# Kernel tuning notes

Hardware: AMD Instinct MI355X
Metric: run time of the kernel (lower is better)

The kernel has to match this reference:

```python
import jax, jax.numpy as jnp
import numpy as np

D = 18          # belief dimension (max category dim)
EPS = 0.1       # C.eps
PROP_STEP = 5   # C.prop_step
CC = 0.01       # label-injection constant c in forward
DIM_A = 4       # category_dim_dict['author']
DIM_P = 18      # category_dim_dict['paper']


def _init_belief(mask, label, dim, d):
    # X[tr_idx] = -c everywhere, then X[tr_idx, label] += dim*c
    m = (mask != 0).astype(jnp.float32)[:, None]            # [N,1]
    X = -CC * m + (dim * CC) * m * jax.nn.one_hot(label, d, dtype=jnp.float32)
    col_mask = (jnp.arange(d) < dim).astype(jnp.float32)    # zero cols >= dim
    Y = X * col_mask
    return X, Y, col_mask


def setup_inputs() -> dict:
    key = jax.random.key(0)
    ks = jax.random.split(key, 8)
    E, NA, NP = 2_000_000, 100_000, 500_000
    return {
        "H_ap": jax.random.normal(ks[0], (D, D), dtype=jnp.float32),
        "H_pa": jax.random.normal(ks[1], (D, D), dtype=jnp.float32),
        "w": jnp.ones((E,), dtype=jnp.float32),
        "edge_src": jax.random.randint(ks[2], (E,), 0, NA, dtype=jnp.int32),
        "edge_dst": jax.random.randint(ks[3], (E,), 0, NP, dtype=jnp.int32),
        "train_mask_a": jax.random.randint(ks[4], (NA,), 0, 2, dtype=jnp.int32),
        "label_a": jax.random.randint(ks[5], (NA,), 0, DIM_A, dtype=jnp.int32),
        "train_mask_p": jax.random.randint(ks[6], (NP,), 0, 2, dtype=jnp.int32),
        "label_p": jax.random.randint(ks[7], (NP,), 0, DIM_P, dtype=jnp.int32),
        "n_author": NA,
        "n_paper": NP,
    }


def reference(H_ap, H_pa, w, edge_src, edge_dst, train_mask_a, label_a,
              train_mask_p, label_p, n_author, n_paper):
    # Belief init via scatter-based label injection (per node type)
    Xa, Ya, cm_a = _init_belief(train_mask_a, label_a, DIM_A, D)
    Xp, Yp, cm_p = _init_belief(train_mask_p, label_p, DIM_P, D)

    seg = jax.ops.segment_sum
    for _ in range(PROP_STEP):  # ZooBP residual updates over hetero edge types
        # author -> paper: gather, transform by H_ap, weighted scatter-add
        msg_p = seg(w[:, None] * (Ya[edge_src] @ H_ap), edge_dst,
                    num_segments=n_paper)                       # [NP, D]
        # paper -> author (inverse etype, H_pa ~ H_ap^T structure)
        msg_a = seg(w[:, None] * (Yp[edge_dst] @ H_pa), edge_src,
                    num_segments=n_author)                      # [NA, D]
        Ya = (Xa + (EPS / D) * msg_a) * cm_a
        Yp = (Xp + (EPS / D) * msg_p) * cm_p
    return Ya, Yp
```

## Files before the change

kernel.cpp:

```cpp
#include <hip/hip_runtime.h>


static constexpr int   DD     = 18;
static constexpr int   DIMA   = 4;
static constexpr float CCF    = 0.01f;
static constexpr float SCALEF = 0.1f / 18.0f;
static constexpr int   PROP   = 5;

static constexpr int NBLK  = 1024;
static constexpr int PBK   = 1024;
static constexpr int ABK   = 512;
static constexpr int NBIN  = PBK + ABK;
static constexpr int NBINS = NBIN * NBLK;

__device__ __forceinline__ float bf2f(unsigned short u) {
    return __uint_as_float(((unsigned int)u) << 16);
}
__device__ __forceinline__ unsigned short f2bf(float f) {
    unsigned int x = __float_as_uint(f);
    return (unsigned short)((x + 0x7fffu + ((x >> 16) & 1u)) >> 16);
}
__device__ __forceinline__ unsigned int f2w13(float f) {
    unsigned int x = __float_as_uint(f);
    return ((x + 0x3ffffu + ((x >> 19) & 1u)) >> 19) & 0x1fffu;
}
__device__ __forceinline__ float w132f(unsigned int u) {
    return __uint_as_float(u << 19);
}
__device__ __forceinline__ int swz_blk() {
    return ((int)blockIdx.x & 7) * (NBLK >> 3) + ((int)blockIdx.x >> 3);
}

__global__ __launch_bounds__(256) void count_bins(
    const int* __restrict__ esrc, const int* __restrict__ edst,
    int* __restrict__ bb, int E, int chunk)
{
    __shared__ int hP[PBK];
    __shared__ int hA[ABK];
    int t = threadIdx.x, b = swz_blk();
    for (int i = t; i < PBK; i += 256) hP[i] = 0;
    for (int i = t; i < ABK; i += 256) hA[i] = 0;
    __syncthreads();
    int beg = b * chunk;
    int end = beg + chunk; if (end > E) end = E;
    for (int e = beg + t; e < end; e += 256) {
        atomicAdd(&hP[edst[e] >> 9], 1);
        atomicAdd(&hA[esrc[e] >> 8], 1);
    }
    __syncthreads();
    for (int i = t; i < PBK; i += 256) bb[i * NBLK + b] = hP[i];
    for (int i = t; i < ABK; i += 256) bb[(PBK + i) * NBLK + b] = hA[i];
}

__global__ __launch_bounds__(256) void scan_block(
    int* __restrict__ off, int* __restrict__ bsum, int NT)
{
    __shared__ int s[256];
    int t = threadIdx.x;
    int i = blockIdx.x * 256 + t;
    int v = (i < NT) ? off[i] : 0;
    s[t] = v; __syncthreads();
    for (int dlt = 1; dlt < 256; dlt <<= 1) {
        int x = (t >= dlt) ? s[t - dlt] : 0;
        __syncthreads();
        s[t] += x;
        __syncthreads();
    }
    if (i < NT) off[i] = s[t] - v;
    if (t == 255) bsum[blockIdx.x] = s[255];
}

__global__ __launch_bounds__(256) void scan_tops(int* __restrict__ bsum, int nb)
{
    __shared__ int s[256];
    int t = threadIdx.x;
    int K = (nb + 255) / 256;
    int base = t * K;
    int sum = 0;
    for (int r = 0; r < K; ++r) { int idx = base + r; if (idx < nb) sum += bsum[idx]; }
    s[t] = sum; __syncthreads();
    for (int dlt = 1; dlt < 256; dlt <<= 1) {
        int x = (t >= dlt) ? s[t - dlt] : 0;
        __syncthreads();
        s[t] += x;
        __syncthreads();
    }
    int run = s[t] - sum;
    for (int r = 0; r < K; ++r) {
        int idx = base + r;
        if (idx < nb) { int tmp = bsum[idx]; bsum[idx] = run; run += tmp; }
    }
}

__global__ __launch_bounds__(256) void scan_add(
    int* __restrict__ off, const int* __restrict__ bsum, int NT, int twoE)
{
    int i = blockIdx.x * 256 + threadIdx.x;
    if (i < NT)       off[i] += bsum[i >> 8];
    else if (i == NT) off[NT] = twoE;
}

__global__ __launch_bounds__(256) void scat_p(
    const int* __restrict__ esrc, const int* __restrict__ edst,
    const float* __restrict__ w, const int* __restrict__ bb,
    uint2* __restrict__ S, int E, int chunk)
{
    __shared__ int base[PBK];
    int t = threadIdx.x, b = swz_blk();
    for (int i = t; i < PBK; i += 256) base[i] = bb[i * NBLK + b];
    __syncthreads();
    int beg = b * chunk;
    int end = beg + chunk; if (end > E) end = E;
    for (int e = beg + t; e < end; e += 256) {
        int d = edst[e], s = esrc[e];
        unsigned int rec = ((unsigned int)s << 13) | f2w13(w[e]);
        int pos = atomicAdd(&base[d >> 9], 1);
        S[pos] = make_uint2(rec, (unsigned int)(d & 511));
    }
}

__global__ __launch_bounds__(256) void scat_a(
    const int* __restrict__ esrc, const int* __restrict__ edst,
    const float* __restrict__ w, const int* __restrict__ bb,
    uint2* __restrict__ S, int E, int chunk)
{
    __shared__ int base[ABK];
    int t = threadIdx.x, b = swz_blk();
    for (int i = t; i < ABK; i += 256) base[i] = bb[(PBK + i) * NBLK + b] - E;
    __syncthreads();
    int beg = b * chunk;
    int end = beg + chunk; if (end > E) end = E;
    for (int e = beg + t; e < end; e += 256) {
        int d = edst[e], s = esrc[e];
        unsigned int rec = ((unsigned int)d << 13) | f2w13(w[e]);
        int pos = atomicAdd(&base[s >> 8], 1);
        S[pos] = make_uint2(rec, (unsigned int)(s & 255));
    }
}

__global__ __launch_bounds__(256) void csr_p(
    const int* __restrict__ bb, const uint2* __restrict__ S,
    unsigned int* __restrict__ adjP, int* __restrict__ offP, int NP, int E)
{
    __shared__ int c[512];
    __shared__ int loc[512];
    __shared__ int ps[256];
    int t = threadIdx.x, b = blockIdx.x;
    int sbeg = bb[b * NBLK];
    int send = bb[(b + 1) * NBLK];
    c[t] = 0; c[t + 256] = 0;
    __syncthreads();
    for (int i = sbeg + t; i < send; i += 256)
        atomicAdd(&c[S[i].y], 1);
    __syncthreads();
    int a0 = c[2 * t], a1 = c[2 * t + 1];
    ps[t] = a0 + a1;
    __syncthreads();
    for (int dlt = 1; dlt < 256; dlt <<= 1) {
        int x = (t >= dlt) ? ps[t - dlt] : 0;
        __syncthreads();
        ps[t] += x;
        __syncthreads();
    }
    int ex = ps[t] - a0 - a1;
    loc[2 * t] = ex;
    loc[2 * t + 1] = ex + a0;
    int n0 = (b << 9) + 2 * t;
    if (n0 < NP)     offP[n0]     = sbeg + ex;
    if (n0 + 1 < NP) offP[n0 + 1] = sbeg + ex + a0;
    if (b == 0 && t == 0) offP[NP] = E;
    __syncthreads();
    for (int i = sbeg + t; i < send; i += 256) {
        uint2 r = S[i];
        int p = atomicAdd(&loc[r.y], 1);
        adjP[sbeg + p] = r.x;
    }
}

__global__ __launch_bounds__(256) void csr_a(
    const int* __restrict__ bb, const uint2* __restrict__ S,
    unsigned int* __restrict__ adjA, int* __restrict__ offA, int NA, int E)
{
    __shared__ int c[256];
    __shared__ int loc[256];
    __shared__ int ps[256];
    int t = threadIdx.x, b = blockIdx.x;
    int sbeg = bb[(PBK + b) * NBLK] - E;
    int send = bb[(PBK + b + 1) * NBLK] - E;
    c[t] = 0;
    __syncthreads();
    for (int i = sbeg + t; i < send; i += 256)
        atomicAdd(&c[S[i].y], 1);
    __syncthreads();
    int a0 = c[t];
    ps[t] = a0;
    __syncthreads();
    for (int dlt = 1; dlt < 256; dlt <<= 1) {
        int x = (t >= dlt) ? ps[t - dlt] : 0;
        __syncthreads();
        ps[t] += x;
        __syncthreads();
    }
    int ex = ps[t] - a0;
    loc[t] = ex;
    int n = (b << 8) + t;
    if (n < NA) offA[n] = sbeg + ex;
    if (b == 0 && t == 0) offA[NA] = E;
    __syncthreads();
    for (int i = sbeg + t; i < send; i += 256) {
        uint2 r = S[i];
        int p = atomicAdd(&loc[r.y], 1);
        adjA[sbeg + p] = r.x;
    }
}

__global__ __launch_bounds__(256) void init_belief(
    const int* __restrict__ mask_a, const int* __restrict__ lab_a,
    const int* __restrict__ mask_p, const int* __restrict__ lab_p,
    const float* __restrict__ Hpa,
    ushort4* __restrict__ Ya, ushort4* __restrict__ Zp,
    unsigned char* __restrict__ priorA, unsigned char* __restrict__ priorP,
    int NA, int NT)
{
    __shared__ float sH[72], sCol[4];
    int t = threadIdx.x;
    if (t < 72) sH[t] = Hpa[(t >> 2) * DD + (t & 3)];
    if (t < 4) { float s = 0.f; for (int k = 0; k < DD; ++k) s += Hpa[k * DD + t]; sCol[t] = s; }
    __syncthreads();
    int i = (int)blockIdx.x * 256 + t;
    if (i >= NT) return;
    if (i < NA) {
        float x[4] = {0.f, 0.f, 0.f, 0.f};
        int m = mask_a[i];
        int l = m ? lab_a[i] : 0;
        if (m) {
            x[0] = x[1] = x[2] = x[3] = -CCF;
            x[l] += (float)DIMA * CCF;
        }
        priorA[i] = m ? (unsigned char)(0x20 | l) : 0;
        Ya[i] = make_ushort4(f2bf(x[0]), f2bf(x[1]), f2bf(x[2]), f2bf(x[3]));
    } else {
        int d = i - NA;
        float z0 = 0.f, z1 = 0.f, z2 = 0.f, z3 = 0.f;
        int m = mask_p[d];
        int l = m ? lab_p[d] : 0;
        if (m) {
            float lb = (float)DD * CCF;
            z0 = -CCF * sCol[0] + lb * sH[l * 4 + 0];
            z1 = -CCF * sCol[1] + lb * sH[l * 4 + 1];
            z2 = -CCF * sCol[2] + lb * sH[l * 4 + 2];
            z3 = -CCF * sCol[3] + lb * sH[l * 4 + 3];
        }
        priorP[d] = m ? (unsigned char)(0x20 | l) : 0;
        Zp[d] = make_ushort4(f2bf(z0), f2bf(z1), f2bf(z2), f2bf(z3));
    }
}

__global__ __launch_bounds__(256) void gather_iter(
    const int* __restrict__ offP, const int* __restrict__ offA,
    const unsigned int* __restrict__ adjP, const unsigned int* __restrict__ adjA,
    const ushort4* __restrict__ ZpOld, ushort4* __restrict__ ZpNew,
    const ushort4* __restrict__ YaOld, ushort4* __restrict__ YaNew,
    const unsigned char* __restrict__ priorA, const unsigned char* __restrict__ priorP,
    const float* __restrict__ Hap, const float* __restrict__ Hpa,
    float* __restrict__ out, int NP, int NA, int last, int gpB)
{
    if ((int)blockIdx.x < gpB) {
        __shared__ float sH[72], sCol[4], sM[16], sHap[72];
        int t = threadIdx.x;
        if (t < 72) sH[t] = Hpa[(t >> 2) * DD + (t & 3)];
        if (t < 4) { float s = 0.f; for (int k = 0; k < DD; ++k) s += Hpa[k * DD + t]; sCol[t] = s; }
        if (t < 16) { int i = t >> 2, j = t & 3; float s = 0.f;
                      for (int k = 0; k < DD; ++k) s += Hap[i * DD + k] * Hpa[k * DD + j];
                      sM[t] = SCALEF * s; }
        if (t < 72) sHap[t] = SCALEF * Hap[t];
        __syncthreads();

        int d = (int)blockIdx.x * 256 + t;
        if (d >= NP) return;
        int beg = offP[d], end = offP[d + 1];
        float ax = 0.f, ay = 0.f, az = 0.f, aw = 0.f;
        int s = beg;
        for (; s + 4 <= end; s += 4) {
            unsigned int e0 = adjP[s], e1 = adjP[s + 1], e2 = adjP[s + 2], e3 = adjP[s + 3];
            ushort4 y0 = YaOld[e0 >> 13], y1 = YaOld[e1 >> 13];
            ushort4 y2 = YaOld[e2 >> 13], y3 = YaOld[e3 >> 13];
            float w0 = w132f(e0 & 0x1fffu), w1 = w132f(e1 & 0x1fffu);
            float w2 = w132f(e2 & 0x1fffu), w3 = w132f(e3 & 0x1fffu);
            ax += w0 * bf2f(y0.x) + w1 * bf2f(y1.x) + w2 * bf2f(y2.x) + w3 * bf2f(y3.x);
            ay += w0 * bf2f(y0.y) + w1 * bf2f(y1.y) + w2 * bf2f(y2.y) + w3 * bf2f(y3.y);
            az += w0 * bf2f(y0.z) + w1 * bf2f(y1.z) + w2 * bf2f(y2.z) + w3 * bf2f(y3.z);
            aw += w0 * bf2f(y0.w) + w1 * bf2f(y1.w) + w2 * bf2f(y2.w) + w3 * bf2f(y3.w);
        }
        for (; s < end; ++s) {
            unsigned int ent = adjP[s];
            float wt = w132f(ent & 0x1fffu);
            ushort4 yv = YaOld[ent >> 13];
            ax += wt * bf2f(yv.x); ay += wt * bf2f(yv.y);
            az += wt * bf2f(yv.z); aw += wt * bf2f(yv.w);
        }
        unsigned int pb = priorP[d];
        int l = pb & 31;
        float base = pb ? -CCF : 0.f;
        float lb   = pb ? (float)DD * CCF : 0.f;
        float z0 = base * sCol[0] + lb * sH[l * 4 + 0] + ax * sM[0] + ay * sM[4] + az * sM[8]  + aw * sM[12];
        float z1 = base * sCol[1] + lb * sH[l * 4 + 1] + ax * sM[1] + ay * sM[5] + az * sM[9]  + aw * sM[13];
        float z2 = base * sCol[2] + lb * sH[l * 4 + 2] + ax * sM[2] + ay * sM[6] + az * sM[10] + aw * sM[14];
        float z3 = base * sCol[3] + lb * sH[l * 4 + 3] + ax * sM[3] + ay * sM[7] + az * sM[11] + aw * sM[15];
        ZpNew[d] = make_ushort4(f2bf(z0), f2bf(z1), f2bf(z2), f2bf(z3));

        if (last) {
            float* row = out + (size_t)(NA + d) * DD;
#pragma unroll
            for (int j = 0; j < DD; ++j) {
                row[j] = base + ((j == l) ? lb : 0.f)
                       + ax * sHap[0 * DD + j] + ay * sHap[1 * DD + j]
                       + az * sHap[2 * DD + j] + aw * sHap[3 * DD + j];
            }
        }
    } else {
        int tid = ((int)blockIdx.x - gpB) * 256 + threadIdx.x;
        int a = tid >> 2, sub = tid & 3;
        if (a >= NA) return;
        int beg = offA[a], end = offA[a + 1];
        float ax = 0.f, ay = 0.f, az = 0.f, aw = 0.f;
        int s = beg + sub;
        for (; s + 4 < end; s += 8) {
            unsigned int e0 = adjA[s], e1 = adjA[s + 4];
            ushort4 z0 = ZpOld[e0 >> 13], z1 = ZpOld[e1 >> 13];
            float w0 = w132f(e0 & 0x1fffu), w1 = w132f(e1 & 0x1fffu);
            ax += w0 * bf2f(z0.x) + w1 * bf2f(z1.x);
            ay += w0 * bf2f(z0.y) + w1 * bf2f(z1.y);
            az += w0 * bf2f(z0.z) + w1 * bf2f(z1.z);
            aw += w0 * bf2f(z0.w) + w1 * bf2f(z1.w);
        }
        if (s < end) {
            unsigned int ent = adjA[s];
            float wt = w132f(ent & 0x1fffu);
            ushort4 z = ZpOld[ent >> 13];
            ax += wt * bf2f(z.x); ay += wt * bf2f(z.y);
            az += wt * bf2f(z.z); aw += wt * bf2f(z.w);
        }
        ax += __shfl_xor(ax, 1); ay += __shfl_xor(ay, 1);
        az += __shfl_xor(az, 1); aw += __shfl_xor(aw, 1);
        ax += __shfl_xor(ax, 2); ay += __shfl_xor(ay, 2);
        az += __shfl_xor(az, 2); aw += __shfl_xor(aw, 2);
        if (sub == 0) {
            unsigned int pb = priorA[a];
            int l = pb & 31;
            float x0 = pb ? ((l == 0) ? ((float)DIMA - 1.f) * CCF : -CCF) : 0.f;
            float x1 = pb ? ((l == 1) ? ((float)DIMA - 1.f) * CCF : -CCF) : 0.f;
            float x2 = pb ? ((l == 2) ? ((float)DIMA - 1.f) * CCF : -CCF) : 0.f;
            float x3 = pb ? ((l == 3) ? ((float)DIMA - 1.f) * CCF : -CCF) : 0.f;
            float y0 = x0 + SCALEF * ax, y1 = x1 + SCALEF * ay;
            float y2 = x2 + SCALEF * az, y3 = x3 + SCALEF * aw;
            YaNew[a] = make_ushort4(f2bf(y0), f2bf(y1), f2bf(y2), f2bf(y3));
            if (last) {
                float* row = out + (size_t)a * DD;
                row[0] = y0; row[1] = y1; row[2] = y2; row[3] = y3;
#pragma unroll
                for (int j = DIMA; j < DD; ++j) row[j] = 0.f;
            }
        }
    }
}

extern "C" void kernel_launch(void* const* d_in, const int* in_sizes, int n_in,
                              void* d_out, int out_size, void* d_ws, size_t ws_size,
                              hipStream_t stream)
{
    const float* H_ap   = (const float*)d_in[0];
    const float* H_pa   = (const float*)d_in[1];
    const float* w      = (const float*)d_in[2];
    const int*   esrc   = (const int*)d_in[3];
    const int*   edst   = (const int*)d_in[4];
    const int*   mask_a = (const int*)d_in[5];
    const int*   lab_a  = (const int*)d_in[6];
    const int*   mask_p = (const int*)d_in[7];
    const int*   lab_p  = (const int*)d_in[8];

    const int E  = in_sizes[2];
    const int NA = in_sizes[5];
    const int NP = in_sizes[7];
    const int NT = NP + NA;

    char*  basep = (char*)d_ws;
    size_t o = 0;
    auto alloc = [&](size_t bytes) -> char* {
        o = (o + 15) & ~(size_t)15;
        char* p = basep + o;
        o += bytes;
        return p;
    };
    int*           offP   = (int*)          alloc((size_t)(NP + 1) * sizeof(int));
    int*           offA   = (int*)          alloc((size_t)(NA + 1) * sizeof(int));
    int*           bb     = (int*)          alloc((size_t)(NBINS + 1) * sizeof(int));
    int*           bsum   = (int*)          alloc((size_t)8192 * sizeof(int));
    unsigned int*  adjP   = (unsigned int*) alloc((size_t)E * sizeof(unsigned int));
    unsigned int*  adjA   = (unsigned int*) alloc((size_t)E * sizeof(unsigned int));
    unsigned char* priorP = (unsigned char*)alloc((size_t)NP);
    unsigned char* priorA = (unsigned char*)alloc((size_t)NA);
    size_t s_bytes  = (size_t)E * sizeof(uint2);
    size_t bl_bytes = (size_t)(2 * NA + 2 * NP) * sizeof(ushort4);
    char*  Sreg = alloc(s_bytes > bl_bytes ? s_bytes : bl_bytes);
    uint2* S    = (uint2*)Sreg;
    ushort4* YaA = (ushort4*)Sreg;
    ushort4* YaB = YaA + NA;
    ushort4* ZpA = YaB + NA;
    ushort4* ZpB = ZpA + NP;
    (void)ws_size;

    float* out = (float*)d_out;
    ushort4* YaBuf[2] = {YaA, YaB};
    ushort4* ZpBuf[2] = {ZpA, ZpB};

    dim3 blk(256);
    const int chunk = (E + NBLK - 1) / NBLK;
    const int gp    = (NP + 255) / 256;
    const int ga4   = (NA * 4 + 255) / 256;
    const int gni   = (NT + 255) / 256;
    const int nb    = (NBINS + 255) / 256;
    const int gnb1  = (NBINS + 1 + 255) / 256;

    count_bins<<<NBLK, blk, 0, stream>>>(esrc, edst, bb, E, chunk);
    scan_block<<<nb, blk, 0, stream>>>(bb, bsum, NBINS);
    scan_tops<<<1, blk, 0, stream>>>(bsum, nb);
    scan_add<<<gnb1, blk, 0, stream>>>(bb, bsum, NBINS, 2 * E);
    scat_p<<<NBLK, blk, 0, stream>>>(esrc, edst, w, bb, S, E, chunk);
    csr_p<<<PBK, blk, 0, stream>>>(bb, S, adjP, offP, NP, E);
    scat_a<<<NBLK, blk, 0, stream>>>(esrc, edst, w, bb, S, E, chunk);
    csr_a<<<ABK, blk, 0, stream>>>(bb, S, adjA, offA, NA, E);
    init_belief<<<gni, blk, 0, stream>>>(mask_a, lab_a, mask_p, lab_p, H_pa,
                                         YaA, ZpA, priorA, priorP, NA, NT);

    for (int it = 0; it < PROP; ++it) {
        int last = (it == PROP - 1) ? 1 : 0;
        int cur = it & 1, nxt = 1 - cur;
        gather_iter<<<gp + ga4, blk, 0, stream>>>(offP, offA, adjP, adjA,
                                                  ZpBuf[cur], ZpBuf[nxt],
                                                  YaBuf[cur], YaBuf[nxt],
                                                  priorA, priorP,
                                                  H_ap, H_pa, out,
                                                  NP, NA, last, gp);
    }
}
```

Before: 381.7 us.

## Coarsen CSR build bins, fold scan_add into consumers, unroll author gather

Each bucket in the two-level counting sort now covers more nodes (2048 papers, 512 authors) and the partition uses half as many blocks, which shrinks the bin-count array and the scan. The separate scan_add kernel is removed; the scatter and CSR kernels add the block prefix sums inline when they read offsets. The author-side gather loop is unrolled to four outstanding loads per thread. The trade-off is more per-bucket work and shared-memory atomics in the csr kernels, plus more contention on the atomic bucket cursors.

```diff
diff --git a/kernel.cpp b/kernel.cpp
--- a/kernel.cpp
+++ b/kernel.cpp
@@ -7,9 +7,13 @@
 static constexpr float SCALEF = 0.1f / 18.0f;
 static constexpr int   PROP   = 5;
 
-static constexpr int NBLK  = 1024;
-static constexpr int PBK   = 1024;
-static constexpr int ABK   = 512;
+static constexpr int NBLK  = 512;
+static constexpr int PSH   = 11;
+static constexpr int ASH   = 9;
+static constexpr int PBK   = 256;
+static constexpr int ABK   = 256;
+static constexpr int PNB   = 1 << PSH;
+static constexpr int ANB   = 1 << ASH;
 static constexpr int NBIN  = PBK + ABK;
 static constexpr int NBINS = NBIN * NBLK;
 
@@ -38,18 +42,18 @@
     __shared__ int hP[PBK];
     __shared__ int hA[ABK];
     int t = threadIdx.x, b = swz_blk();
-    for (int i = t; i < PBK; i += 256) hP[i] = 0;
-    for (int i = t; i < ABK; i += 256) hA[i] = 0;
+    if (t < PBK) hP[t] = 0;
+    if (t < ABK) hA[t] = 0;
     __syncthreads();
     int beg = b * chunk;
     int end = beg + chunk; if (end > E) end = E;
     for (int e = beg + t; e < end; e += 256) {
-        atomicAdd(&hP[edst[e] >> 9], 1);
-        atomicAdd(&hA[esrc[e] >> 8], 1);
-    }
-    __syncthreads();
-    for (int i = t; i < PBK; i += 256) bb[i * NBLK + b] = hP[i];
-    for (int i = t; i < ABK; i += 256) bb[(PBK + i) * NBLK + b] = hA[i];
+        atomicAdd(&hP[edst[e] >> PSH], 1);
+        atomicAdd(&hA[esrc[e] >> ASH], 1);
+    }
+    __syncthreads();
+    if (t < PBK) bb[t * NBLK + b] = hP[t];
+    if (t < ABK) bb[(PBK + t) * NBLK + b] = hA[t];
 }
 
 __global__ __launch_bounds__(256) void scan_block(
@@ -92,82 +96,86 @@
     }
 }
 
-__global__ __launch_bounds__(256) void scan_add(
-    int* __restrict__ off, const int* __restrict__ bsum, int NT, int twoE)
-{
-    int i = blockIdx.x * 256 + threadIdx.x;
-    if (i < NT)       off[i] += bsum[i >> 8];
-    else if (i == NT) off[NT] = twoE;
-}
-
 __global__ __launch_bounds__(256) void scat_p(
     const int* __restrict__ esrc, const int* __restrict__ edst,
     const float* __restrict__ w, const int* __restrict__ bb,
-    uint2* __restrict__ S, int E, int chunk)
+    const int* __restrict__ bsum, uint2* __restrict__ S, int E, int chunk)
 {
     __shared__ int base[PBK];
     int t = threadIdx.x, b = swz_blk();
-    for (int i = t; i < PBK; i += 256) base[i] = bb[i * NBLK + b];
+    if (t < PBK) {
+        int idx = t * NBLK + b;
+        base[t] = bb[idx] + bsum[idx >> 8];
+    }
     __syncthreads();
     int beg = b * chunk;
     int end = beg + chunk; if (end > E) end = E;
     for (int e = beg + t; e < end; e += 256) {
         int d = edst[e], s = esrc[e];
         unsigned int rec = ((unsigned int)s << 13) | f2w13(w[e]);
-        int pos = atomicAdd(&base[d >> 9], 1);
-        S[pos] = make_uint2(rec, (unsigned int)(d & 511));
+        int pos = atomicAdd(&base[d >> PSH], 1);
+        S[pos] = make_uint2(rec, (unsigned int)(d & (PNB - 1)));
     }
 }
 
 __global__ __launch_bounds__(256) void scat_a(
     const int* __restrict__ esrc, const int* __restrict__ edst,
     const float* __restrict__ w, const int* __restrict__ bb,
-    uint2* __restrict__ S, int E, int chunk)
+    const int* __restrict__ bsum, uint2* __restrict__ S, int E, int chunk)
 {
     __shared__ int base[ABK];
     int t = threadIdx.x, b = swz_blk();
-    for (int i = t; i < ABK; i += 256) base[i] = bb[(PBK + i) * NBLK + b] - E;
+    if (t < ABK) {
+        int idx = (PBK + t) * NBLK + b;
+        base[t] = bb[idx] + bsum[idx >> 8] - E;
+    }
     __syncthreads();
     int beg = b * chunk;
     int end = beg + chunk; if (end > E) end = E;
     for (int e = beg + t; e < end; e += 256) {
         int d = edst[e], s = esrc[e];
         unsigned int rec = ((unsigned int)d << 13) | f2w13(w[e]);
-        int pos = atomicAdd(&base[s >> 8], 1);
-        S[pos] = make_uint2(rec, (unsigned int)(s & 255));
+        int pos = atomicAdd(&base[s >> ASH], 1);
+        S[pos] = make_uint2(rec, (unsigned int)(s & (ANB - 1)));
     }
 }
 
 __global__ __launch_bounds__(256) void csr_p(
-    const int* __restrict__ bb, const uint2* __restrict__ S,
+    const int* __restrict__ bb, const int* __restrict__ bsum,
+    const uint2* __restrict__ S,
     unsigned int* __restrict__ adjP, int* __restrict__ offP, int NP, int E)
 {
-    __shared__ int c[512];
-    __shared__ int loc[512];
+    __shared__ int c[PNB];
+    __shared__ int loc[PNB];
     __shared__ int ps[256];
     int t = threadIdx.x, b = blockIdx.x;
-    int sbeg = bb[b * NBLK];
-    int send = bb[(b + 1) * NBLK];
-    c[t] = 0; c[t + 256] = 0;
+    int i0 = b * NBLK;
+    int i1 = (b + 1) * NBLK;
+    int sbeg = bb[i0] + bsum[i0 >> 8];
+    int send = bb[i1] + bsum[i1 >> 8];
+    for (int i = t; i < PNB; i += 256) c[i] = 0;
     __syncthreads();
     for (int i = sbeg + t; i < send; i += 256)
         atomicAdd(&c[S[i].y], 1);
     __syncthreads();
-    int a0 = c[2 * t], a1 = c[2 * t + 1];
-    ps[t] = a0 + a1;
-    __syncthreads();
+    int a[8]; int sum = 0;
+#pragma unroll
+    for (int k = 0; k < 8; ++k) { a[k] = c[t * 8 + k]; sum += a[k]; }
+    ps[t] = sum; __syncthreads();
     for (int dlt = 1; dlt < 256; dlt <<= 1) {
         int x = (t >= dlt) ? ps[t - dlt] : 0;
         __syncthreads();
         ps[t] += x;
         __syncthreads();
     }
-    int ex = ps[t] - a0 - a1;
-    loc[2 * t] = ex;
-    loc[2 * t + 1] = ex + a0;
-    int n0 = (b << 9) + 2 * t;
-    if (n0 < NP)     offP[n0]     = sbeg + ex;
-    if (n0 + 1 < NP) offP[n0 + 1] = sbeg + ex + a0;
+    int run = ps[t] - sum;
+    int n0 = (b << PSH) + t * 8;
+#pragma unroll
+    for (int k = 0; k < 8; ++k) {
+        loc[t * 8 + k] = run;
+        if (n0 + k < NP) offP[n0 + k] = sbeg + run;
+        run += a[k];
+    }
     if (b == 0 && t == 0) offP[NP] = E;
     __syncthreads();
     for (int i = sbeg + t; i < send; i += 256) {
@@ -178,22 +186,26 @@
 }
 
 __global__ __launch_bounds__(256) void csr_a(
-    const int* __restrict__ bb, const uint2* __restrict__ S,
+    const int* __restrict__ bb, const int* __restrict__ bsum,
+    const uint2* __restrict__ S,
     unsigned int* __restrict__ adjA, int* __restrict__ offA, int NA, int E)
 {
-    __shared__ int c[256];
-    __shared__ int loc[256];
+    __shared__ int c[ANB];
+    __shared__ int loc[ANB];
     __shared__ int ps[256];
     int t = threadIdx.x, b = blockIdx.x;
-    int sbeg = bb[(PBK + b) * NBLK] - E;
-    int send = bb[(PBK + b + 1) * NBLK] - E;
-    c[t] = 0;
+    int x0 = (PBK + b) * NBLK;
+    int sbeg = bb[x0] + bsum[x0 >> 8] - E;
+    int send;
+    if (b == ABK - 1) send = E;
+    else { int x1 = x0 + NBLK; send = bb[x1] + bsum[x1 >> 8] - E; }
+    c[t] = 0; c[t + 256] = 0;
     __syncthreads();
     for (int i = sbeg + t; i < send; i += 256)
         atomicAdd(&c[S[i].y], 1);
     __syncthreads();
-    int a0 = c[t];
-    ps[t] = a0;
+    int a0 = c[2 * t], a1 = c[2 * t + 1];
+    ps[t] = a0 + a1;
     __syncthreads();
     for (int dlt = 1; dlt < 256; dlt <<= 1) {
         int x = (t >= dlt) ? ps[t - dlt] : 0;
@@ -201,10 +213,12 @@
         ps[t] += x;
         __syncthreads();
     }
-    int ex = ps[t] - a0;
-    loc[t] = ex;
-    int n = (b << 8) + t;
-    if (n < NA) offA[n] = sbeg + ex;
+    int ex = ps[t] - a0 - a1;
+    loc[2 * t] = ex;
+    loc[2 * t + 1] = ex + a0;
+    int n0 = (b << ASH) + 2 * t;
+    if (n0 < NA)     offA[n0]     = sbeg + ex;
+    if (n0 + 1 < NA) offA[n0 + 1] = sbeg + ex + a0;
     if (b == 0 && t == 0) offA[NA] = E;
     __syncthreads();
     for (int i = sbeg + t; i < send; i += 256) {
@@ -325,16 +339,18 @@
         int beg = offA[a], end = offA[a + 1];
         float ax = 0.f, ay = 0.f, az = 0.f, aw = 0.f;
         int s = beg + sub;
-        for (; s + 4 < end; s += 8) {
-            unsigned int e0 = adjA[s], e1 = adjA[s + 4];
+        for (; s + 12 < end; s += 16) {
+            unsigned int e0 = adjA[s], e1 = adjA[s + 4], e2 = adjA[s + 8], e3 = adjA[s + 12];
             ushort4 z0 = ZpOld[e0 >> 13], z1 = ZpOld[e1 >> 13];
+            ushort4 z2 = ZpOld[e2 >> 13], z3 = ZpOld[e3 >> 13];
             float w0 = w132f(e0 & 0x1fffu), w1 = w132f(e1 & 0x1fffu);
-            ax += w0 * bf2f(z0.x) + w1 * bf2f(z1.x);
-            ay += w0 * bf2f(z0.y) + w1 * bf2f(z1.y);
-            az += w0 * bf2f(z0.z) + w1 * bf2f(z1.z);
-            aw += w0 * bf2f(z0.w) + w1 * bf2f(z1.w);
-        }
-        if (s < end) {
+            float w2 = w132f(e2 & 0x1fffu), w3 = w132f(e3 & 0x1fffu);
+            ax += w0 * bf2f(z0.x) + w1 * bf2f(z1.x) + w2 * bf2f(z2.x) + w3 * bf2f(z3.x);
+            ay += w0 * bf2f(z0.y) + w1 * bf2f(z1.y) + w2 * bf2f(z2.y) + w3 * bf2f(z3.y);
+            az += w0 * bf2f(z0.z) + w1 * bf2f(z1.z) + w2 * bf2f(z2.z) + w3 * bf2f(z3.z);
+            aw += w0 * bf2f(z0.w) + w1 * bf2f(z1.w) + w2 * bf2f(z2.w) + w3 * bf2f(z3.w);
+        }
+        for (; s < end; s += 4) {
             unsigned int ent = adjA[s];
             float wt = w132f(ent & 0x1fffu);
             ushort4 z = ZpOld[ent >> 13];
@@ -395,7 +411,7 @@
     int*           offP   = (int*)          alloc((size_t)(NP + 1) * sizeof(int));
     int*           offA   = (int*)          alloc((size_t)(NA + 1) * sizeof(int));
     int*           bb     = (int*)          alloc((size_t)(NBINS + 1) * sizeof(int));
-    int*           bsum   = (int*)          alloc((size_t)8192 * sizeof(int));
+    int*           bsum   = (int*)          alloc((size_t)4096 * sizeof(int));
     unsigned int*  adjP   = (unsigned int*) alloc((size_t)E * sizeof(unsigned int));
     unsigned int*  adjA   = (unsigned int*) alloc((size_t)E * sizeof(unsigned int));
     unsigned char* priorP = (unsigned char*)alloc((size_t)NP);
@@ -420,16 +436,14 @@
     const int ga4   = (NA * 4 + 255) / 256;
     const int gni   = (NT + 255) / 256;
     const int nb    = (NBINS + 255) / 256;
-    const int gnb1  = (NBINS + 1 + 255) / 256;
 
     count_bins<<<NBLK, blk, 0, stream>>>(esrc, edst, bb, E, chunk);
     scan_block<<<nb, blk, 0, stream>>>(bb, bsum, NBINS);
     scan_tops<<<1, blk, 0, stream>>>(bsum, nb);
-    scan_add<<<gnb1, blk, 0, stream>>>(bb, bsum, NBINS, 2 * E);
-    scat_p<<<NBLK, blk, 0, stream>>>(esrc, edst, w, bb, S, E, chunk);
-    csr_p<<<PBK, blk, 0, stream>>>(bb, S, adjP, offP, NP, E);
-    scat_a<<<NBLK, blk, 0, stream>>>(esrc, edst, w, bb, S, E, chunk);
-    csr_a<<<ABK, blk, 0, stream>>>(bb, S, adjA, offA, NA, E);
+    scat_p<<<NBLK, blk, 0, stream>>>(esrc, edst, w, bb, bsum, S, E, chunk);
+    csr_p<<<PBK, blk, 0, stream>>>(bb, bsum, S, adjP, offP, NP, E);
+    scat_a<<<NBLK, blk, 0, stream>>>(esrc, edst, w, bb, bsum, S, E, chunk);
+    csr_a<<<ABK, blk, 0, stream>>>(bb, bsum, S, adjA, offA, NA, E);
     init_belief<<<gni, blk, 0, stream>>>(mask_a, lab_a, mask_p, lab_p, H_pa,
                                          YaA, ZpA, priorA, priorP, NA, NT);
 
```

New measurement: 372.3 us. -2.5%, faster.
